# Kernel optimization log

Hardware: AMD Instinct MI355X
Metric: run time of the kernel (lower is better)

## Reference

```python
import jax, jax.numpy as jnp
import numpy as np

B, S, D, H = 2, 2048, 1024, 16
DK = D // H  # 64


def setup_inputs() -> dict:
    key = jax.random.key(0)
    ks = jax.random.split(key, 11)
    scale = 1.0 / np.sqrt(D)
    inp = {
        "x": jax.random.normal(ks[0], (B, S, D), dtype=jnp.float32),
        "z": jax.random.normal(ks[1], (B, S, D), dtype=jnp.float32),
        # causal mask, broadcast over batch and heads; masked_fill where mask==0
        "mask": jnp.tril(jnp.ones((1, 1, S, S), dtype=jnp.int32)),
        "wq_w": jax.random.normal(ks[2], (D, D), dtype=jnp.float32) * scale,
        "wq_b": jax.random.normal(ks[3], (D,), dtype=jnp.float32) * 0.01,
        "wk_w": jax.random.normal(ks[4], (D, D), dtype=jnp.float32) * scale,
        "wk_b": jax.random.normal(ks[5], (D,), dtype=jnp.float32) * 0.01,
        "wv_w": jax.random.normal(ks[6], (D, D), dtype=jnp.float32) * scale,
        "wv_b": jax.random.normal(ks[7], (D,), dtype=jnp.float32) * 0.01,
        "wo_w": jax.random.normal(ks[8], (D, D), dtype=jnp.float32) * scale,
        "wo_b": jax.random.normal(ks[9], (D,), dtype=jnp.float32) * 0.01,
    }
    return inp


def reference(x, z, mask, wq_w, wq_b, wk_w, wk_b, wv_w, wv_b, wo_w, wo_b):
    # torch Linear: y = x @ W.T + b
    q = x @ wq_w.T + wq_b
    k = z @ wk_w.T + wk_b
    # NOTE: faithful to source bug: value uses wk, not wv (wv is a dead param)
    v = z @ wk_w.T + wk_b

    def split_heads(t):  # [B,S,D] -> [B,H,S,DK]
        return t.reshape(B, S, H, DK).transpose(0, 2, 1, 3)

    q, k, v = split_heads(q), split_heads(k), split_heads(v)

    scores = jnp.einsum("bhqd,bhkd->bhqk", q, k) * (DK ** -0.5)
    scores = jnp.where(mask == 0, -jnp.inf, scores)
    attn_weights = jax.nn.softmax(scores, axis=-1)  # [B,H,S,S]
    atn = jnp.einsum("bhqk,bhkd->bhqd", attn_weights, v)

    concat = atn.transpose(0, 2, 1, 3).reshape(B, S, D)
    output = concat @ wo_w.T + wo_b  # dropout rate 0.0 -> identity
    concat_attn_weight = attn_weights.sum(axis=1)  # [B,S,S]
    return output, concat_attn_weight
```

## Files before the change

kernel.cpp:

```cpp
#include <hip/hip_runtime.h>

typedef __bf16 bf16_t;
typedef __bf16 bf16x4 __attribute__((ext_vector_type(4)));
typedef __bf16 bf16x8 __attribute__((ext_vector_type(8)));
typedef float  f32x4  __attribute__((ext_vector_type(4)));

#define MFMA(a, b, c) __builtin_amdgcn_mfma_f32_16x16x32_bf16((a), (b), (c), 0, 0, 0)

static constexpr int Bsz = 2, S = 2048, D = 1024, H = 16, DK = 64;

__device__ __forceinline__ bf16x8 pack8(float4 a, float4 b) {
    bf16x8 r;
    r[0] = (bf16_t)a.x; r[1] = (bf16_t)a.y; r[2] = (bf16_t)a.z; r[3] = (bf16_t)a.w;
    r[4] = (bf16_t)b.x; r[5] = (bf16_t)b.y; r[6] = (bf16_t)b.z; r[7] = (bf16_t)b.w;
    return r;
}

__global__ __launch_bounds__(512) void gemm_qk(
    const float* __restrict__ xA, const float* __restrict__ wqB,
    const float* __restrict__ wqb, bf16_t* __restrict__ Qc,
    const float* __restrict__ zA, const float* __restrict__ wkB,
    const float* __restrict__ wkb, bf16_t* __restrict__ Kc,
    bf16_t* __restrict__ KTout)
{
    constexpr int M = Bsz * S, N = D, K = D;
    const int zi = blockIdx.z;
    const float* A    = zi ? zA  : xA;
    const float* B    = zi ? wkB : wqB;
    const float* bias = zi ? wkb : wqb;
    bf16_t*      C    = zi ? Kc  : Qc;
    const float  sc   = zi ? 1.f : 0.125f;

    __shared__ bf16_t As[2][128][40];
    __shared__ bf16_t Bs[2][128][40];

    const int t    = threadIdx.x;
    const int wave = t >> 6, lane = t & 63;
    const int quad = lane >> 4, l15 = lane & 15;
    const int wm = (wave >> 1) * 32, wn = (wave & 1) * 64;
    const int rowbase = blockIdx.y * 128, colbase = blockIdx.x * 128;
    const int r  = t >> 2;
    const int cc = (t & 3) << 3;

    f32x4 acc[2][4];
#pragma unroll
    for (int i = 0; i < 2; ++i)
#pragma unroll
        for (int j = 0; j < 4; ++j) acc[i][j] = {0.f, 0.f, 0.f, 0.f};

    float4 a0 = *(const float4*)&A[(size_t)(rowbase + r) * K + cc];
    float4 a1 = *(const float4*)&A[(size_t)(rowbase + r) * K + cc + 4];
    float4 b0 = *(const float4*)&B[(size_t)(colbase + r) * K + cc];
    float4 b1 = *(const float4*)&B[(size_t)(colbase + r) * K + cc + 4];
    *(bf16x8*)&As[0][r][cc] = pack8(a0, a1);
    *(bf16x8*)&Bs[0][r][cc] = pack8(b0, b1);
    __syncthreads();

    for (int kt = 0; kt < K; kt += 32) {
        const int cur = (kt >> 5) & 1, nxt = cur ^ 1;
        const bool more = (kt + 32) < K;
        if (more) {
            a0 = *(const float4*)&A[(size_t)(rowbase + r) * K + kt + 32 + cc];
            a1 = *(const float4*)&A[(size_t)(rowbase + r) * K + kt + 32 + cc + 4];
            b0 = *(const float4*)&B[(size_t)(colbase + r) * K + kt + 32 + cc];
            b1 = *(const float4*)&B[(size_t)(colbase + r) * K + kt + 32 + cc + 4];
        }

        bf16x8 af[2], bfr[4];
#pragma unroll
        for (int mt = 0; mt < 2; ++mt)
            af[mt] = *(const bf16x8*)&As[cur][wm + mt * 16 + l15][quad * 8];
#pragma unroll
        for (int nt = 0; nt < 4; ++nt)
            bfr[nt] = *(const bf16x8*)&Bs[cur][wn + nt * 16 + l15][quad * 8];
#pragma unroll
        for (int mt = 0; mt < 2; ++mt)
#pragma unroll
            for (int nt = 0; nt < 4; ++nt)
                acc[mt][nt] = MFMA(af[mt], bfr[nt], acc[mt][nt]);

        if (more) {
            *(bf16x8*)&As[nxt][r][cc] = pack8(a0, a1);
            *(bf16x8*)&Bs[nxt][r][cc] = pack8(b0, b1);
        }
        __syncthreads();
    }

#pragma unroll
    for (int nt = 0; nt < 4; ++nt) {
        int col  = colbase + wn + nt * 16 + l15;
        float bv = bias[col];
#pragma unroll
        for (int mt = 0; mt < 2; ++mt) {
            int row0 = rowbase + wm + mt * 16 + quad * 4;
#pragma unroll
            for (int rr = 0; rr < 4; ++rr) {
                float v = (acc[mt][nt][rr] + bv) * sc;
                C[(size_t)(row0 + rr) * N + col] = (bf16_t)v;
                if (zi) {
                    int row = row0 + rr;
                    int bb = row >> 11, srow = row & (S - 1);
                    int hh = col >> 6,  dd   = col & 63;
                    KTout[(((size_t)bb * H + hh) * DK + dd) * S + srow] = (bf16_t)v;
                }
            }
        }
    }
}

__global__ __launch_bounds__(512) void gemm_obt(
    const bf16_t* __restrict__ A, const float* __restrict__ B,
    const float* __restrict__ bias, float* __restrict__ C)
{
    constexpr int M = Bsz * S, N = D, K = D;
    __shared__ bf16_t As[2][128][40];
    __shared__ bf16_t Bs[2][128][40];

    const int t    = threadIdx.x;
    const int wave = t >> 6, lane = t & 63;
    const int quad = lane >> 4, l15 = lane & 15;
    const int wm = (wave >> 1) * 32, wn = (wave & 1) * 64;
    const int rowbase = blockIdx.y * 128, colbase = blockIdx.x * 128;
    const int r  = t >> 2;
    const int cc = (t & 3) << 3;

    f32x4 acc[2][4];
#pragma unroll
    for (int i = 0; i < 2; ++i)
#pragma unroll
        for (int j = 0; j < 4; ++j) acc[i][j] = {0.f, 0.f, 0.f, 0.f};

    bf16x8 areg = *(const bf16x8*)&A[(size_t)(rowbase + r) * K + cc];
    float4 b0   = *(const float4*)&B[(size_t)(colbase + r) * K + cc];
    float4 b1   = *(const float4*)&B[(size_t)(colbase + r) * K + cc + 4];
    *(bf16x8*)&As[0][r][cc] = areg;
    *(bf16x8*)&Bs[0][r][cc] = pack8(b0, b1);
    __syncthreads();

    for (int kt = 0; kt < K; kt += 32) {
        const int cur = (kt >> 5) & 1, nxt = cur ^ 1;
        const bool more = (kt + 32) < K;
        if (more) {
            areg = *(const bf16x8*)&A[(size_t)(rowbase + r) * K + kt + 32 + cc];
            b0   = *(const float4*)&B[(size_t)(colbase + r) * K + kt + 32 + cc];
            b1   = *(const float4*)&B[(size_t)(colbase + r) * K + kt + 32 + cc + 4];
        }

        bf16x8 af[2], bfr[4];
#pragma unroll
        for (int mt = 0; mt < 2; ++mt)
            af[mt] = *(const bf16x8*)&As[cur][wm + mt * 16 + l15][quad * 8];
#pragma unroll
        for (int nt = 0; nt < 4; ++nt)
            bfr[nt] = *(const bf16x8*)&Bs[cur][wn + nt * 16 + l15][quad * 8];
#pragma unroll
        for (int mt = 0; mt < 2; ++mt)
#pragma unroll
            for (int nt = 0; nt < 4; ++nt)
                acc[mt][nt] = MFMA(af[mt], bfr[nt], acc[mt][nt]);

        if (more) {
            *(bf16x8*)&As[nxt][r][cc] = areg;
            *(bf16x8*)&Bs[nxt][r][cc] = pack8(b0, b1);
        }
        __syncthreads();
    }

#pragma unroll
    for (int nt = 0; nt < 4; ++nt) {
        int col  = colbase + wn + nt * 16 + l15;
        float bv = bias[col];
#pragma unroll
        for (int mt = 0; mt < 2; ++mt) {
            int row0 = rowbase + wm + mt * 16 + quad * 4;
#pragma unroll
            for (int rr = 0; rr < 4; ++rr)
                C[(size_t)(row0 + rr) * N + col] = acc[mt][nt][rr] + bv;
        }
    }
}

__global__ __launch_bounds__(256) void attn_flash(
    const bf16_t* __restrict__ Q, const bf16_t* __restrict__ Km,
    const bf16_t* __restrict__ KT,
    bf16_t* __restrict__ Oc, float* __restrict__ m_ws, float* __restrict__ il_ws)
{
    const int h = blockIdx.y, b = blockIdx.z;
    const int t = threadIdx.x;
    const int wave = t >> 6, lane = t & 63;
    const int quad = lane >> 4, l15 = lane & 15;

    __shared__ bf16_t Ks[2][64][72];
    __shared__ bf16_t KTs[2][64][72];
    __shared__ bf16_t PQ[64][72];

    const int hcol = h * DK;
    const bf16_t* KTh = KT + ((size_t)(b * H + h)) * DK * S;
    const size_t bS = (size_t)b * S;

    const int jr = (t >> 3);
    const int ce = (t & 7) * 8;
    const int iloc = wave * 16 + l15;

    for (int half = 0; half < 2; ++half) {
        const int qt = half == 0 ? (int)blockIdx.x : 31 - (int)blockIdx.x;
        const size_t qrow0 = bS + (size_t)qt * 64;

        __syncthreads();
        bf16x8 qld[2], kreg[2], ktreg[2];
#pragma unroll
        for (int p = 0; p < 2; ++p) {
            qld[p]   = *(const bf16x8*)&Q[(qrow0 + p * 32 + jr) * D + hcol + ce];
            kreg[p]  = *(const bf16x8*)&Km[(bS + p * 32 + jr) * D + hcol + ce];
            ktreg[p] = *(const bf16x8*)&KTh[(size_t)(p * 32 + jr) * S + ce];
        }
#pragma unroll
        for (int p = 0; p < 2; ++p) {
            *(bf16x8*)&PQ[p * 32 + jr][ce]     = qld[p];
            *(bf16x8*)&Ks[0][p * 32 + jr][ce]  = kreg[p];
            *(bf16x8*)&KTs[0][p * 32 + jr][ce] = ktreg[p];
        }
        __syncthreads();
        const bf16x8 qf0 = *(const bf16x8*)&PQ[wave * 16 + l15][quad * 8];
        const bf16x8 qf1 = *(const bf16x8*)&PQ[wave * 16 + l15][32 + quad * 8];

        f32x4 accO[4];
#pragma unroll
        for (int u = 0; u < 4; ++u) accO[u] = {0.f, 0.f, 0.f, 0.f};
        float m_cur = -1e30f, l_cur = 0.f;

        auto softmax_pv = [&](f32x4 sv[4], int cur) {
            float tm = sv[0][0];
#pragma unroll
            for (int nt = 0; nt < 4; ++nt)
#pragma unroll
                for (int r = 0; r < 4; ++r) tm = fmaxf(tm, sv[nt][r]);
            tm = fmaxf(tm, __shfl_xor(tm, 16));
            tm = fmaxf(tm, __shfl_xor(tm, 32));
            float m_new = fmaxf(m_cur, tm);
            float alpha = __expf(m_cur - m_new);
            m_cur = m_new;
            float rs = 0.f;
#pragma unroll
            for (int nt = 0; nt < 4; ++nt)
#pragma unroll
                for (int r = 0; r < 4; ++r) {
                    float p = __expf(sv[nt][r] - m_new);
                    sv[nt][r] = p;
                    rs += p;
                }
            rs += __shfl_xor(rs, 16);
            rs += __shfl_xor(rs, 32);
            l_cur = l_cur * alpha + rs;

            float alpha4[4];
#pragma unroll
            for (int r = 0; r < 4; ++r)
                alpha4[r] = __shfl(alpha, (quad << 4) + quad * 4 + r, 64);
#pragma unroll
            for (int u = 0; u < 4; ++u)
#pragma unroll
                for (int r = 0; r < 4; ++r) accO[u][r] *= alpha4[r];

#pragma unroll
            for (int nt = 0; nt < 4; ++nt) {
                bf16x4 pk;
                pk[0] = (bf16_t)sv[nt][0]; pk[1] = (bf16_t)sv[nt][1];
                pk[2] = (bf16_t)sv[nt][2]; pk[3] = (bf16_t)sv[nt][3];
                *(bf16x4*)&PQ[wave * 16 + l15][nt * 16 + quad * 4] = pk;
            }
            asm volatile("s_waitcnt lgkmcnt(0)" ::: "memory");

            bf16x8 pa0 = *(const bf16x8*)&PQ[wave * 16 + l15][quad * 8];
            bf16x8 pa1 = *(const bf16x8*)&PQ[wave * 16 + l15][32 + quad * 8];
#pragma unroll
            for (int u = 0; u < 4; ++u) {
                bf16x8 v0 = *(const bf16x8*)&KTs[cur][u * 16 + l15][quad * 8];
                bf16x8 v1 = *(const bf16x8*)&KTs[cur][u * 16 + l15][32 + quad * 8];
                accO[u] = MFMA(pa0, v0, accO[u]);
                accO[u] = MFMA(pa1, v1, accO[u]);
            }
        };

        for (int jt = 0; jt < qt; ++jt) {
            const int cur = jt & 1, nxt = cur ^ 1;
#pragma unroll
            for (int p = 0; p < 2; ++p) {
                kreg[p]  = *(const bf16x8*)&Km[(bS + (size_t)(jt + 1) * 64 + p * 32 + jr) * D + hcol + ce];
                ktreg[p] = *(const bf16x8*)&KTh[(size_t)(p * 32 + jr) * S + (size_t)(jt + 1) * 64 + ce];
            }

            f32x4 sv[4];
#pragma unroll
            for (int nt = 0; nt < 4; ++nt) {
                bf16x8 a0 = *(const bf16x8*)&Ks[cur][nt * 16 + l15][quad * 8];
                bf16x8 a1 = *(const bf16x8*)&Ks[cur][nt * 16 + l15][32 + quad * 8];
                f32x4 a = {0.f, 0.f, 0.f, 0.f};
                a = MFMA(a0, qf0, a);
                a = MFMA(a1, qf1, a);
                sv[nt] = a;
            }
            softmax_pv(sv, cur);

#pragma unroll
            for (int p = 0; p < 2; ++p) {
                *(bf16x8*)&Ks[nxt][p * 32 + jr][ce]  = kreg[p];
                *(bf16x8*)&KTs[nxt][p * 32 + jr][ce] = ktreg[p];
            }
            __syncthreads();
        }

        {
            const int cur = qt & 1;
            f32x4 sv[4];
#pragma unroll
            for (int nt = 0; nt < 4; ++nt) {
                bf16x8 a0 = *(const bf16x8*)&Ks[cur][nt * 16 + l15][quad * 8];
                bf16x8 a1 = *(const bf16x8*)&Ks[cur][nt * 16 + l15][32 + quad * 8];
                f32x4 a = {0.f, 0.f, 0.f, 0.f};
                a = MFMA(a0, qf0, a);
                a = MFMA(a1, qf1, a);
#pragma unroll
                for (int r = 0; r < 4; ++r)
                    if ((nt * 16 + quad * 4 + r) > iloc) a[r] = -1e30f;
                sv[nt] = a;
            }
            softmax_pv(sv, cur);
        }

        float invl = 1.f / l_cur;
        float invl4[4];
#pragma unroll
        for (int r = 0; r < 4; ++r)
            invl4[r] = __shfl(invl, (quad << 4) + quad * 4 + r, 64);
#pragma unroll
        for (int u = 0; u < 4; ++u)
#pragma unroll
            for (int r = 0; r < 4; ++r)
                Oc[(qrow0 + wave * 16 + quad * 4 + r) * D + hcol + u * 16 + l15] =
                    (bf16_t)(accO[u][r] * invl4[r]);

        if (quad == 0) {
            size_t sb = ((size_t)(b * H + h)) * S + (size_t)qt * 64 + wave * 16 + l15;
            m_ws[sb]  = m_cur;
            il_ws[sb] = invl;
        }
    }
}

__global__ __launch_bounds__(256) void attn_wsum(
    const bf16_t* __restrict__ Q, const bf16_t* __restrict__ Km,
    const float* __restrict__ m_ws, const float* __restrict__ il_ws,
    float* __restrict__ out2)
{
    const int jt = blockIdx.x, qt = blockIdx.y, b = blockIdx.z;
    const int t  = threadIdx.x;
    float* tile = out2 + (size_t)b * S * S + (size_t)qt * 64 * S + (size_t)jt * 64;

    if (jt > qt) {
        int r0 = t >> 2, c0 = (t & 3) * 16;
#pragma unroll
        for (int e = 0; e < 16; ++e) tile[(size_t)r0 * S + c0 + e] = 0.f;
        return;
    }

    const int wave = t >> 6, lane = t & 63;
    const int quad = lane >> 4, l15 = lane & 15;
    __shared__ bf16_t Ks[2][64][72];
    __shared__ bf16_t Qs[2][64][72];

    const int jr = (t >> 3), ce = (t & 7) * 8;
    const size_t krow = (size_t)b * S + (size_t)jt * 64;
    const size_t qrow = (size_t)b * S + (size_t)qt * 64;

    f32x4 accs[4];
#pragma unroll
    for (int nt = 0; nt < 4; ++nt) accs[nt] = {0.f, 0.f, 0.f, 0.f};

    bf16x8 kreg[2], qreg[2];
#pragma unroll
    for (int p = 0; p < 2; ++p) {
        kreg[p] = *(const bf16x8*)&Km[(krow + p * 32 + jr) * D + ce];
        qreg[p] = *(const bf16x8*)&Q[(qrow + p * 32 + jr) * D + ce];
    }
#pragma unroll
    for (int p = 0; p < 2; ++p) {
        *(bf16x8*)&Ks[0][p * 32 + jr][ce] = kreg[p];
        *(bf16x8*)&Qs[0][p * 32 + jr][ce] = qreg[p];
    }
    __syncthreads();

    for (int h = 0; h < H; ++h) {
        const int cur = h & 1, nxt = cur ^ 1;

        if (h < H - 1) {
            const int hc = (h + 1) * DK;
#pragma unroll
            for (int p = 0; p < 2; ++p) {
                kreg[p] = *(const bf16x8*)&Km[(krow + p * 32 + jr) * D + hc + ce];
                qreg[p] = *(const bf16x8*)&Q[(qrow + p * 32 + jr) * D + hc + ce];
            }
        }

        bf16x8 qf0 = *(const bf16x8*)&Qs[cur][wave * 16 + l15][quad * 8];
        bf16x8 qf1 = *(const bf16x8*)&Qs[cur][wave * 16 + l15][32 + quad * 8];

        size_t mlb = ((size_t)(b * H + h)) * S + (size_t)qt * 64 + wave * 16 + quad * 4;
        f32x4 mr = *(const f32x4*)&m_ws[mlb];
        f32x4 il = *(const f32x4*)&il_ws[mlb];

#pragma unroll
        for (int nt = 0; nt < 4; ++nt) {
            bf16x8 k0 = *(const bf16x8*)&Ks[cur][nt * 16 + l15][quad * 8];
            bf16x8 k1 = *(const bf16x8*)&Ks[cur][nt * 16 + l15][32 + quad * 8];
            f32x4 a = {0.f, 0.f, 0.f, 0.f};
            a = MFMA(qf0, k0, a);
            a = MFMA(qf1, k1, a);
#pragma unroll
            for (int r = 0; r < 4; ++r) {
                int i = qt * 64 + wave * 16 + quad * 4 + r;
                int j = jt * 64 + nt * 16 + l15;
                float p = (j <= i) ? __expf(a[r] - mr[r]) * il[r] : 0.f;
                accs[nt][r] += p;
            }
        }

        if (h < H - 1) {
#pragma unroll
            for (int p = 0; p < 2; ++p) {
                *(bf16x8*)&Ks[nxt][p * 32 + jr][ce] = kreg[p];
                *(bf16x8*)&Qs[nxt][p * 32 + jr][ce] = qreg[p];
            }
        }
        __syncthreads();
    }

#pragma unroll
    for (int nt = 0; nt < 4; ++nt)
#pragma unroll
        for (int r = 0; r < 4; ++r)
            tile[(size_t)(wave * 16 + quad * 4 + r) * S + nt * 16 + l15] = accs[nt][r];
}

extern "C" void kernel_launch(void* const* d_in, const int* in_sizes, int n_in,
                              void* d_out, int out_size, void* d_ws, size_t ws_size,
                              hipStream_t stream)
{
    const float* x    = (const float*)d_in[0];
    const float* z    = (const float*)d_in[1];
    const float* wq_w = (const float*)d_in[3];
    const float* wq_b = (const float*)d_in[4];
    const float* wk_w = (const float*)d_in[5];
    const float* wk_b = (const float*)d_in[6];
    const float* wo_w = (const float*)d_in[9];
    const float* wo_b = (const float*)d_in[10];

    float* out  = (float*)d_out;
    float* out2 = out + (size_t)Bsz * S * D;

    float*  m_ws  = (float*)d_ws;
    float*  il_ws = m_ws + (size_t)Bsz * H * S;
    bf16_t* Qws   = (bf16_t*)(il_ws + (size_t)Bsz * H * S);
    bf16_t* Kws   = Qws + (size_t)Bsz * S * D;
    bf16_t* Cc    = (bf16_t*)out2;
    bf16_t* KTws  = Cc + (size_t)Bsz * S * D;

    gemm_qk<<<dim3(D / 128, (Bsz * S) / 128, 2), dim3(512), 0, stream>>>(
        x, wq_w, wq_b, Qws, z, wk_w, wk_b, Kws, KTws);
    attn_flash<<<dim3(S / 128, H, Bsz), dim3(256), 0, stream>>>(
        Qws, Kws, KTws, Cc, m_ws, il_ws);
    gemm_obt<<<dim3(D / 128, (Bsz * S) / 128, 1), dim3(512), 0, stream>>>(
        Cc, wo_w, wo_b, out);
    attn_wsum<<<dim3(S / 64, S / 64, Bsz), dim3(256), 0, stream>>>(
        Qws, Kws, m_ws, il_ws, out2);
}
```

Baseline: 286.8 us.

## Pre-convert inputs and weights to bf16 once; halve output GEMM tile rows

Adds a single conversion kernel that casts x, z and the Q/K/O weights to bf16 up front, storing x and z in scratch space inside the output buffer. The GEMMs then load bf16 directly instead of loading fp32 and packing inside the main loop, which was done redundantly by every tile that reads the same data. The output projection GEMM also moves to 64-row tiles with 256 threads, doubling its block count to improve occupancy. The cost is an extra launch and a full read-convert-write pass over the inputs and weights.

```diff
diff --git a/kernel.cpp b/kernel.cpp
--- a/kernel.cpp
+++ b/kernel.cpp
@@ -9,27 +9,42 @@
 
 static constexpr int Bsz = 2, S = 2048, D = 1024, H = 16, DK = 64;
 
-__device__ __forceinline__ bf16x8 pack8(float4 a, float4 b) {
-    bf16x8 r;
-    r[0] = (bf16_t)a.x; r[1] = (bf16_t)a.y; r[2] = (bf16_t)a.z; r[3] = (bf16_t)a.w;
-    r[4] = (bf16_t)b.x; r[5] = (bf16_t)b.y; r[6] = (bf16_t)b.z; r[7] = (bf16_t)b.w;
-    return r;
+__global__ __launch_bounds__(256) void cvt5(
+    const float* __restrict__ x, const float* __restrict__ z,
+    const float* __restrict__ wq, const float* __restrict__ wk,
+    const float* __restrict__ wo,
+    bf16_t* __restrict__ xb, bf16_t* __restrict__ zb,
+    bf16_t* __restrict__ wqb, bf16_t* __restrict__ wkb, bf16_t* __restrict__ wob)
+{
+    constexpr int NXZ = Bsz * S * D / 4;
+    constexpr int NW  = D * D / 4;
+    int i = blockIdx.x * 256 + threadIdx.x;
+    const float* s; bf16_t* d; int off;
+    if (i < NXZ)                 { s = x;  d = xb;  off = i; }
+    else if (i < 2 * NXZ)        { s = z;  d = zb;  off = i - NXZ; }
+    else if (i < 2 * NXZ + NW)   { s = wq; d = wqb; off = i - 2 * NXZ; }
+    else if (i < 2 * NXZ + 2*NW) { s = wk; d = wkb; off = i - 2 * NXZ - NW; }
+    else                         { s = wo; d = wob; off = i - 2 * NXZ - 2 * NW; }
+    float4 v = *(const float4*)&s[(size_t)off * 4];
+    bf16x4 o;
+    o[0] = (bf16_t)v.x; o[1] = (bf16_t)v.y; o[2] = (bf16_t)v.z; o[3] = (bf16_t)v.w;
+    *(bf16x4*)&d[(size_t)off * 4] = o;
 }
 
 __global__ __launch_bounds__(512) void gemm_qk(
-    const float* __restrict__ xA, const float* __restrict__ wqB,
+    const bf16_t* __restrict__ xA, const bf16_t* __restrict__ wqB,
     const float* __restrict__ wqb, bf16_t* __restrict__ Qc,
-    const float* __restrict__ zA, const float* __restrict__ wkB,
+    const bf16_t* __restrict__ zA, const bf16_t* __restrict__ wkB,
     const float* __restrict__ wkb, bf16_t* __restrict__ Kc,
     bf16_t* __restrict__ KTout)
 {
-    constexpr int M = Bsz * S, N = D, K = D;
+    constexpr int N = D, K = D;
     const int zi = blockIdx.z;
-    const float* A    = zi ? zA  : xA;
-    const float* B    = zi ? wkB : wqB;
-    const float* bias = zi ? wkb : wqb;
-    bf16_t*      C    = zi ? Kc  : Qc;
-    const float  sc   = zi ? 1.f : 0.125f;
+    const bf16_t* A    = zi ? zA  : xA;
+    const bf16_t* B    = zi ? wkB : wqB;
+    const float*  bias = zi ? wkb : wqb;
+    bf16_t*       C    = zi ? Kc  : Qc;
+    const float   sc   = zi ? 1.f : 0.125f;
 
     __shared__ bf16_t As[2][128][40];
     __shared__ bf16_t Bs[2][128][40];
@@ -48,22 +63,18 @@
 #pragma unroll
         for (int j = 0; j < 4; ++j) acc[i][j] = {0.f, 0.f, 0.f, 0.f};
 
-    float4 a0 = *(const float4*)&A[(size_t)(rowbase + r) * K + cc];
-    float4 a1 = *(const float4*)&A[(size_t)(rowbase + r) * K + cc + 4];
-    float4 b0 = *(const float4*)&B[(size_t)(colbase + r) * K + cc];
-    float4 b1 = *(const float4*)&B[(size_t)(colbase + r) * K + cc + 4];
-    *(bf16x8*)&As[0][r][cc] = pack8(a0, a1);
-    *(bf16x8*)&Bs[0][r][cc] = pack8(b0, b1);
+    bf16x8 areg = *(const bf16x8*)&A[(size_t)(rowbase + r) * K + cc];
+    bf16x8 breg = *(const bf16x8*)&B[(size_t)(colbase + r) * K + cc];
+    *(bf16x8*)&As[0][r][cc] = areg;
+    *(bf16x8*)&Bs[0][r][cc] = breg;
     __syncthreads();
 
     for (int kt = 0; kt < K; kt += 32) {
         const int cur = (kt >> 5) & 1, nxt = cur ^ 1;
         const bool more = (kt + 32) < K;
         if (more) {
-            a0 = *(const float4*)&A[(size_t)(rowbase + r) * K + kt + 32 + cc];
-            a1 = *(const float4*)&A[(size_t)(rowbase + r) * K + kt + 32 + cc + 4];
-            b0 = *(const float4*)&B[(size_t)(colbase + r) * K + kt + 32 + cc];
-            b1 = *(const float4*)&B[(size_t)(colbase + r) * K + kt + 32 + cc + 4];
+            areg = *(const bf16x8*)&A[(size_t)(rowbase + r) * K + kt + 32 + cc];
+            breg = *(const bf16x8*)&B[(size_t)(colbase + r) * K + kt + 32 + cc];
         }
 
         bf16x8 af[2], bfr[4];
@@ -80,8 +91,8 @@
                 acc[mt][nt] = MFMA(af[mt], bfr[nt], acc[mt][nt]);
 
         if (more) {
-            *(bf16x8*)&As[nxt][r][cc] = pack8(a0, a1);
-            *(bf16x8*)&Bs[nxt][r][cc] = pack8(b0, b1);
+            *(bf16x8*)&As[nxt][r][cc] = areg;
+            *(bf16x8*)&Bs[nxt][r][cc] = breg;
         }
         __syncthreads();
     }
@@ -108,19 +119,19 @@
     }
 }
 
-__global__ __launch_bounds__(512) void gemm_obt(
-    const bf16_t* __restrict__ A, const float* __restrict__ B,
+__global__ __launch_bounds__(256) void gemm_obt(
+    const bf16_t* __restrict__ A, const bf16_t* __restrict__ B,
     const float* __restrict__ bias, float* __restrict__ C)
 {
-    constexpr int M = Bsz * S, N = D, K = D;
-    __shared__ bf16_t As[2][128][40];
+    constexpr int N = D, K = D;
+    __shared__ bf16_t As[2][64][40];
     __shared__ bf16_t Bs[2][128][40];
 
     const int t    = threadIdx.x;
     const int wave = t >> 6, lane = t & 63;
     const int quad = lane >> 4, l15 = lane & 15;
     const int wm = (wave >> 1) * 32, wn = (wave & 1) * 64;
-    const int rowbase = blockIdx.y * 128, colbase = blockIdx.x * 128;
+    const int rowbase = blockIdx.y * 64, colbase = blockIdx.x * 128;
     const int r  = t >> 2;
     const int cc = (t & 3) << 3;
 
@@ -131,19 +142,20 @@
         for (int j = 0; j < 4; ++j) acc[i][j] = {0.f, 0.f, 0.f, 0.f};
 
     bf16x8 areg = *(const bf16x8*)&A[(size_t)(rowbase + r) * K + cc];
-    float4 b0   = *(const float4*)&B[(size_t)(colbase + r) * K + cc];
-    float4 b1   = *(const float4*)&B[(size_t)(colbase + r) * K + cc + 4];
-    *(bf16x8*)&As[0][r][cc] = areg;
-    *(bf16x8*)&Bs[0][r][cc] = pack8(b0, b1);
+    bf16x8 breg0 = *(const bf16x8*)&B[(size_t)(colbase + r) * K + cc];
+    bf16x8 breg1 = *(const bf16x8*)&B[(size_t)(colbase + 64 + r) * K + cc];
+    *(bf16x8*)&As[0][r][cc]      = areg;
+    *(bf16x8*)&Bs[0][r][cc]      = breg0;
+    *(bf16x8*)&Bs[0][64 + r][cc] = breg1;
     __syncthreads();
 
     for (int kt = 0; kt < K; kt += 32) {
         const int cur = (kt >> 5) & 1, nxt = cur ^ 1;
         const bool more = (kt + 32) < K;
         if (more) {
-            areg = *(const bf16x8*)&A[(size_t)(rowbase + r) * K + kt + 32 + cc];
-            b0   = *(const float4*)&B[(size_t)(colbase + r) * K + kt + 32 + cc];
-            b1   = *(const float4*)&B[(size_t)(colbase + r) * K + kt + 32 + cc + 4];
+            areg  = *(const bf16x8*)&A[(size_t)(rowbase + r) * K + kt + 32 + cc];
+            breg0 = *(const bf16x8*)&B[(size_t)(colbase + r) * K + kt + 32 + cc];
+            breg1 = *(const bf16x8*)&B[(size_t)(colbase + 64 + r) * K + kt + 32 + cc];
         }
 
         bf16x8 af[2], bfr[4];
@@ -160,8 +172,9 @@
                 acc[mt][nt] = MFMA(af[mt], bfr[nt], acc[mt][nt]);
 
         if (more) {
-            *(bf16x8*)&As[nxt][r][cc] = areg;
-            *(bf16x8*)&Bs[nxt][r][cc] = pack8(b0, b1);
+            *(bf16x8*)&As[nxt][r][cc]      = areg;
+            *(bf16x8*)&Bs[nxt][r][cc]      = breg0;
+            *(bf16x8*)&Bs[nxt][64 + r][cc] = breg1;
         }
         __syncthreads();
     }
@@ -462,15 +475,23 @@
     float*  il_ws = m_ws + (size_t)Bsz * H * S;
     bf16_t* Qws   = (bf16_t*)(il_ws + (size_t)Bsz * H * S);
     bf16_t* Kws   = Qws + (size_t)Bsz * S * D;
+    bf16_t* wq_bf = Kws + (size_t)Bsz * S * D;
+    bf16_t* wk_bf = wq_bf + (size_t)D * D;
+    bf16_t* wo_bf = wk_bf + (size_t)D * D;
+    bf16_t* xb    = (bf16_t*)out;
+    bf16_t* zb    = xb + (size_t)Bsz * S * D;
     bf16_t* Cc    = (bf16_t*)out2;
     bf16_t* KTws  = Cc + (size_t)Bsz * S * D;
 
+    constexpr int CVT_BLOCKS = (2 * (Bsz * S * D / 4) + 3 * (D * D / 4)) / 256;
+    cvt5<<<dim3(CVT_BLOCKS), dim3(256), 0, stream>>>(
+        x, z, wq_w, wk_w, wo_w, xb, zb, wq_bf, wk_bf, wo_bf);
     gemm_qk<<<dim3(D / 128, (Bsz * S) / 128, 2), dim3(512), 0, stream>>>(
-        x, wq_w, wq_b, Qws, z, wk_w, wk_b, Kws, KTws);
+        xb, wq_bf, wq_b, Qws, zb, wk_bf, wk_b, Kws, KTws);
     attn_flash<<<dim3(S / 128, H, Bsz), dim3(256), 0, stream>>>(
         Qws, Kws, KTws, Cc, m_ws, il_ws);
-    gemm_obt<<<dim3(D / 128, (Bsz * S) / 128, 1), dim3(512), 0, stream>>>(
-        Cc, wo_w, wo_b, out);
+    gemm_obt<<<dim3(D / 128, (Bsz * S) / 64, 1), dim3(256), 0, stream>>>(
+        Cc, wo_bf, wo_b, out);
     attn_wsum<<<dim3(S / 64, S / 64, Bsz), dim3(256), 0, stream>>>(
         Qws, Kws, m_ws, il_ws, out2);
 }
```

After: 265.1 us. 7.6% less time.
